# Performance work log

Measured on AMD Instinct MI355X. Metric: run time of the kernel, lower is better.

The kernel has to match this reference:

```python
import jax, jax.numpy as jnp
import numpy as np

B, L, D, H = 2, 2048, 2048, 16
C = D // H  # head dim = 128
EPS = 1e-5


def setup_inputs() -> dict:
    key = jax.random.key(0)
    k1, k2, k3, k4 = jax.random.split(key, 4)
    scale = 1.0 / np.sqrt(D)
    return {
        "x": jax.random.normal(k1, (B, L, D), dtype=jnp.float32),
        "theta": jax.random.uniform(k2, (B, L, D // 2), dtype=jnp.float32) * 6.2831853,
        "w_qkv": jax.random.normal(k3, (3 * D, D), dtype=jnp.float32) * scale,
        "w_y": jax.random.normal(k4, (D, D), dtype=jnp.float32) * scale,
        "b_y": jnp.zeros((D,), dtype=jnp.float32),
    }


def _rms_norm(t):
    # RMSNorm over last dim, eps=1e-5, no affine
    return t * jax.lax.rsqrt(jnp.mean(t * t, axis=-1, keepdims=True) + EPS)


def _apply_rope(q, k, theta):
    # q, k: (B, H, L, C); theta: (B, H, L, C//2)
    qr, qi = q[..., 0::2], q[..., 1::2]
    kr, ki = k[..., 0::2], k[..., 1::2]
    cos_t, sin_t = jnp.cos(theta), jnp.sin(theta)
    q_rot = jnp.stack((qr * cos_t - qi * sin_t, qr * sin_t + qi * cos_t), axis=-1).reshape(q.shape)
    k_rot = jnp.stack((kr * cos_t - ki * sin_t, kr * sin_t + ki * cos_t), axis=-1).reshape(k.shape)
    return q_rot, k_rot


def reference(x, theta, w_qkv, w_y, b_y):
    # QKV projection: (B, L, 3D)
    qkv = jnp.einsum("bld,ed->ble", x, w_qkv)
    # rearrange '... L (n H C) -> n ... H L C'
    qkv = qkv.reshape(B, L, 3, H, C).transpose(2, 0, 3, 1, 4)  # (3, B, H, L, C)
    q, k, v = qkv[0], qkv[1], qkv[2]
    q, k = _rms_norm(q), _rms_norm(k)
    # theta: (B, L, H*C/2) -> (B, H, L, C/2)
    th = theta.reshape(B, L, H, C // 2).transpose(0, 2, 1, 3)
    q, k = _apply_rope(q, k, th)
    # scaled dot-product attention
    scores = jnp.einsum("bhqc,bhkc->bhqk", q, k) / np.sqrt(C).astype(np.float32)
    attn = jax.nn.softmax(scores, axis=-1)
    y = jnp.einsum("bhqk,bhkc->bhqc", attn, v)
    # (B, H, L, C) -> (B, L, H*C)
    y = y.transpose(0, 2, 1, 3).reshape(B, L, D)
    return jnp.einsum("bld,ed->ble", y, w_y) + b_y
```

## Files before the change

kernel.cpp:

```cpp
#include <hip/hip_runtime.h>
#include <stdint.h>

typedef uint16_t u16;
typedef __attribute__((ext_vector_type(8))) short bf16x8;
typedef __attribute__((ext_vector_type(4))) float f32x4;


__device__ __forceinline__ u16 f2bf(float f) {
  uint32_t u = __builtin_bit_cast(uint32_t, f);
  u += 0x7fffu + ((u >> 16) & 1u);
  return (u16)(u >> 16);
}
__device__ __forceinline__ float bf2f(u16 h) {
  return __builtin_bit_cast(float, (uint32_t)h << 16);
}
__device__ __forceinline__ uint32_t pack2bf(float a, float b) {
  uint32_t ua = __builtin_bit_cast(uint32_t, a) + 0x7fffu;
  uint32_t ub = __builtin_bit_cast(uint32_t, b) + 0x7fffu;
  return (ua >> 16) | (ub & 0xffff0000u);
}
__device__ __forceinline__ void gl_lds16(const u16* g, u16* l) {
  __builtin_amdgcn_global_load_lds((const __attribute__((address_space(1))) uint32_t*)g,
                                   (__attribute__((address_space(3))) uint32_t*)l, 16, 0, 0);
}

__global__ __launch_bounds__(256) void cast3(const float* __restrict__ x,
                                             const float* __restrict__ wqkv,
                                             const float* __restrict__ wy,
                                             u16* __restrict__ xb, u16* __restrict__ wqb,
                                             u16* __restrict__ wyb) {
  const int N1 = 2097152, N2 = N1 + 3145728, N3 = N2 + 1048576;
  int stride = gridDim.x * 256;
  for (int i = blockIdx.x * 256 + threadIdx.x; i < N3; i += stride) {
    const float* src;
    u16* dst;
    int off;
    if (i < N1) {
      src = x; dst = xb; off = i;
    } else if (i < N2) {
      src = wqkv; dst = wqb; off = i - N1;
    } else {
      src = wy; dst = wyb; off = i - N2;
    }
    float4 v = *(const float4*)(src + (size_t)off * 4);
    uint32_t lo = (uint32_t)f2bf(v.x) | ((uint32_t)f2bf(v.y) << 16);
    uint32_t hi = (uint32_t)f2bf(v.z) | ((uint32_t)f2bf(v.w) << 16);
    *(uint2*)(dst + (size_t)off * 4) = make_uint2(lo, hi);
  }
}

__global__ __launch_bounds__(512, 1) void gemm8_qkv(
    const u16* __restrict__ A, const u16* __restrict__ Bw,
    u16* __restrict__ qb, u16* __restrict__ kb, u16* __restrict__ vt) {
  __shared__ u16 sm[57344];
  const int K = 2048;
  const int tid = threadIdx.x, lane = tid & 63;
  const int wid = tid >> 6, g = lane >> 4, lr = lane & 15;
  const int wm = wid >> 2, wn = wid & 3;
  const int m0 = blockIdx.y * 256, n0 = blockIdx.x * 192;
  const int srow = tid >> 3, sjs = (tid & 7) ^ (srow & 7);

  auto stA = [&](int buf, int kt, int R) {
    gl_lds16(A + (size_t)(m0 + R + srow) * K + kt * 64 + sjs * 8,
             &sm[buf * 28672 + R * 64 + tid * 8]);
  };
  auto stB = [&](int buf, int kt, int R) {
    gl_lds16(Bw + (size_t)(n0 + R + srow) * K + kt * 64 + sjs * 8,
             &sm[buf * 28672 + 16384 + R * 64 + tid * 8]);
  };
  auto rdA = [&](const u16* As, int mf, int ks) {
    int ra = wm * 128 + mf * 16 + lr;
    return *(const bf16x8*)&As[ra * 64 + (((ks * 4 + g) ^ (ra & 7)) * 8)];
  };
  auto rdB = [&](const u16* Bs, int nf, int ks) {
    int rb = wn * 48 + nf * 16 + lr;
    return *(const bf16x8*)&Bs[rb * 64 + (((ks * 4 + g) ^ (rb & 7)) * 8)];
  };

  f32x4 acc[8][3] = {};
  bf16x8 bc[3][2], fP0[4][2], fP1[4][2];

  stB(0, 0, 0); stB(0, 0, 64); stB(0, 0, 128);
  stA(0, 0, 0); stA(0, 0, 128);
  stA(0, 0, 64); stA(0, 0, 192);
  asm volatile("s_waitcnt vmcnt(2)" ::: "memory");
  __builtin_amdgcn_s_barrier();
  {
    const u16* As0 = &sm[0];
#pragma unroll
    for (int i = 0; i < 4; ++i)
#pragma unroll
      for (int ks = 0; ks < 2; ++ks) fP0[i][ks] = rdA(As0, i, ks);
  }

  for (int t = 0; t < 32; ++t) {
    const int cur = t & 1, nxt = cur ^ 1;
    const int kn = (t < 31) ? t + 1 : 31;
    const u16* Asc = &sm[cur * 28672];
    const u16* Bsc = &sm[cur * 28672 + 16384];
    const u16* Asn = &sm[nxt * 28672];

    stB(nxt, kn, 0); stB(nxt, kn, 64); stB(nxt, kn, 128);
    stA(nxt, kn, 0); stA(nxt, kn, 128);
    asm volatile("s_waitcnt vmcnt(5)" ::: "memory");
    __builtin_amdgcn_s_barrier();
#pragma unroll
    for (int nf = 0; nf < 3; ++nf)
#pragma unroll
      for (int ks = 0; ks < 2; ++ks) bc[nf][ks] = rdB(Bsc, nf, ks);
#pragma unroll
    for (int i = 0; i < 4; ++i)
#pragma unroll
      for (int ks = 0; ks < 2; ++ks) fP1[i][ks] = rdA(Asc, 4 + i, ks);
    __builtin_amdgcn_s_setprio(1);
#pragma unroll
    for (int i = 0; i < 4; ++i)
#pragma unroll
      for (int nf = 0; nf < 3; ++nf) {
        acc[i][nf] = __builtin_amdgcn_mfma_f32_16x16x32_bf16(
            fP0[i][0], bc[nf][0], acc[i][nf], 0, 0, 0);
        acc[i][nf] = __builtin_amdgcn_mfma_f32_16x16x32_bf16(
            fP0[i][1], bc[nf][1], acc[i][nf], 0, 0, 0);
      }
    __builtin_amdgcn_s_setprio(0);

    stA(nxt, kn, 64); stA(nxt, kn, 192);
    asm volatile("s_waitcnt vmcnt(2)" ::: "memory");
    __builtin_amdgcn_s_barrier();
#pragma unroll
    for (int i = 0; i < 4; ++i)
#pragma unroll
      for (int ks = 0; ks < 2; ++ks) fP0[i][ks] = rdA(Asn, i, ks);
    __builtin_amdgcn_s_setprio(1);
#pragma unroll
    for (int i = 0; i < 4; ++i)
#pragma unroll
      for (int nf = 0; nf < 3; ++nf) {
        acc[4 + i][nf] = __builtin_amdgcn_mfma_f32_16x16x32_bf16(
            fP1[i][0], bc[nf][0], acc[4 + i][nf], 0, 0, 0);
        acc[4 + i][nf] = __builtin_amdgcn_mfma_f32_16x16x32_bf16(
            fP1[i][1], bc[nf][1], acc[4 + i][nf], 0, 0, 0);
      }
    __builtin_amdgcn_s_setprio(0);
  }
  asm volatile("s_waitcnt vmcnt(0)" ::: "memory");

#pragma unroll
  for (int mf = 0; mf < 8; ++mf)
#pragma unroll
    for (int nf = 0; nf < 3; ++nf) {
      int n = n0 + wn * 48 + nf * 16 + lr;
      int s = n >> 11, h = (n >> 7) & 15, cb = n & 127;
#pragma unroll
      for (int r = 0; r < 4; ++r) {
        int m = m0 + wm * 128 + mf * 16 + g * 4 + r;
        int b = m >> 11, lp = m & 2047;
        u16 val = f2bf(acc[mf][nf][r]);
        if (s == 0)
          qb[(size_t)((b * 16 + h) * 2048 + lp) * 128 + cb] = val;
        else if (s == 1)
          kb[(size_t)((b * 16 + h) * 2048 + lp) * 128 + cb] = val;
        else
          vt[(size_t)((b * 16 + h) * 128 + cb) * 2048 + lp] = val;
      }
    }
}

__global__ __launch_bounds__(256, 2) void gemm_out(
    const u16* __restrict__ A, const u16* __restrict__ Bw,
    float* __restrict__ out, const float* __restrict__ bias) {
  __shared__ u16 sm[32768];
  const int K = 2048;
  const int tid = threadIdx.x, lane = tid & 63;
  const int wn = tid >> 6, g = lane >> 4, lr = lane & 15;
  const int m0 = blockIdx.y * 128, n0 = blockIdx.x * 128;
  const int srow = tid >> 3, sjs = (tid & 7) ^ (srow & 7);

  auto stA = [&](int buf, int kt, int R) {
    gl_lds16(A + (size_t)(m0 + R + srow) * K + kt * 64 + sjs * 8,
             &sm[buf * 16384 + R * 64 + tid * 8]);
  };
  auto stB = [&](int buf, int kt, int R) {
    gl_lds16(Bw + (size_t)(n0 + R + srow) * K + kt * 64 + sjs * 8,
             &sm[buf * 16384 + 8192 + R * 64 + tid * 8]);
  };
  auto rdA = [&](const u16* As, int mf, int ks) {
    int ra = mf * 16 + lr;
    return *(const bf16x8*)&As[ra * 64 + (((ks * 4 + g) ^ (ra & 7)) * 8)];
  };
  auto rdB = [&](const u16* Bs, int nf, int ks) {
    int rb = wn * 32 + nf * 16 + lr;
    return *(const bf16x8*)&Bs[rb * 64 + (((ks * 4 + g) ^ (rb & 7)) * 8)];
  };

  f32x4 acc[8][2] = {};
  bf16x8 bc[2][2], fP0[4][2], fP1[4][2];

  stB(0, 0, 0); stB(0, 0, 32); stB(0, 0, 64); stB(0, 0, 96);
  stA(0, 0, 0); stA(0, 0, 32);
  stA(0, 0, 64); stA(0, 0, 96);
  asm volatile("s_waitcnt vmcnt(2)" ::: "memory");
  __builtin_amdgcn_s_barrier();
  {
    const u16* As0 = &sm[0];
#pragma unroll
    for (int i = 0; i < 4; ++i)
#pragma unroll
      for (int ks = 0; ks < 2; ++ks) fP0[i][ks] = rdA(As0, i, ks);
  }

  for (int t = 0; t < 32; ++t) {
    const int cur = t & 1, nxt = cur ^ 1;
    const int kn = (t < 31) ? t + 1 : 31;
    const u16* Asc = &sm[cur * 16384];
    const u16* Bsc = &sm[cur * 16384 + 8192];
    const u16* Asn = &sm[nxt * 16384];

    stB(nxt, kn, 0); stB(nxt, kn, 32); stB(nxt, kn, 64); stB(nxt, kn, 96);
    stA(nxt, kn, 0); stA(nxt, kn, 32);
    asm volatile("s_waitcnt vmcnt(6)" ::: "memory");
    __builtin_amdgcn_s_barrier();
#pragma unroll
    for (int nf = 0; nf < 2; ++nf)
#pragma unroll
      for (int ks = 0; ks < 2; ++ks) bc[nf][ks] = rdB(Bsc, nf, ks);
#pragma unroll
    for (int i = 0; i < 4; ++i)
#pragma unroll
      for (int ks = 0; ks < 2; ++ks) fP1[i][ks] = rdA(Asc, 4 + i, ks);
    __builtin_amdgcn_s_setprio(1);
#pragma unroll
    for (int i = 0; i < 4; ++i)
#pragma unroll
      for (int nf = 0; nf < 2; ++nf) {
        acc[i][nf] = __builtin_amdgcn_mfma_f32_16x16x32_bf16(
            fP0[i][0], bc[nf][0], acc[i][nf], 0, 0, 0);
        acc[i][nf] = __builtin_amdgcn_mfma_f32_16x16x32_bf16(
            fP0[i][1], bc[nf][1], acc[i][nf], 0, 0, 0);
      }
    __builtin_amdgcn_s_setprio(0);

    stA(nxt, kn, 64); stA(nxt, kn, 96);
    asm volatile("s_waitcnt vmcnt(2)" ::: "memory");
    __builtin_amdgcn_s_barrier();
#pragma unroll
    for (int i = 0; i < 4; ++i)
#pragma unroll
      for (int ks = 0; ks < 2; ++ks) fP0[i][ks] = rdA(Asn, i, ks);
    __builtin_amdgcn_s_setprio(1);
#pragma unroll
    for (int i = 0; i < 4; ++i)
#pragma unroll
      for (int nf = 0; nf < 2; ++nf) {
        acc[4 + i][nf] = __builtin_amdgcn_mfma_f32_16x16x32_bf16(
            fP1[i][0], bc[nf][0], acc[4 + i][nf], 0, 0, 0);
        acc[4 + i][nf] = __builtin_amdgcn_mfma_f32_16x16x32_bf16(
            fP1[i][1], bc[nf][1], acc[4 + i][nf], 0, 0, 0);
      }
    __builtin_amdgcn_s_setprio(0);
  }
  asm volatile("s_waitcnt vmcnt(0)" ::: "memory");

#pragma unroll
  for (int mf = 0; mf < 8; ++mf)
#pragma unroll
    for (int nf = 0; nf < 2; ++nf) {
      int n = n0 + wn * 32 + nf * 16 + lr;
      float bv = bias[n];
#pragma unroll
      for (int r = 0; r < 4; ++r) {
        int m = m0 + mf * 16 + g * 4 + r;
        out[(size_t)m * 2048 + n] = acc[mf][nf][r] + bv;
      }
    }
}

__global__ __launch_bounds__(256) void k_fix(u16* __restrict__ kb,
                                             const float* __restrict__ theta) {
  const int row = blockIdx.x * 4 + (threadIdx.x >> 6);
  const int lane = threadIdx.x & 63;
  const int bh = row >> 11, l = row & 2047;
  const int b = bh >> 4, h = bh & 15;
  float th = theta[(size_t)(b * 2048 + l) * 1024 + h * 64 + lane];
  float sn, cs;
  __sincosf(th, &sn, &cs);
  uint32_t* p = (uint32_t*)(kb + (size_t)row * 128) + lane;
  uint32_t v = *p;
  float x0 = bf2f((u16)(v & 0xffff)), x1 = bf2f((u16)(v >> 16));
  float ss = x0 * x0 + x1 * x1;
#pragma unroll
  for (int m = 1; m <= 32; m <<= 1) ss += __shfl_xor(ss, m);
  float rn = rsqrtf(ss * (1.0f / 128.0f) + 1e-5f);
  x0 *= rn;
  x1 *= rn;
  float y0 = x0 * cs - x1 * sn;
  float y1 = x0 * sn + x1 * cs;
  *p = (uint32_t)f2bf(y0) | ((uint32_t)f2bf(y1) << 16);
}

__global__ __launch_bounds__(512, 1) void attn_k(const u16* __restrict__ qb,
                                                 const u16* __restrict__ kb,
                                                 const u16* __restrict__ vt,
                                                 const float* __restrict__ theta,
                                                 u16* __restrict__ yb) {
  __shared__ u16 sm[49152];
  const int gid = blockIdx.x;
  const int bh = (gid & 7) * 4 + ((gid >> 3) & 3);
  const int qtile = gid >> 5;
  const int b = bh >> 4, h = bh & 15;
  const int tid = threadIdx.x, lane = tid & 63, wid = tid >> 6;
  const int g = lane >> 4, lr = lane & 15;
  const int q0 = qtile * 256 + wid * 32;

  bf16x8 qf[2][4];
#pragma unroll
  for (int qs = 0; qs < 2; ++qs) {
    const int l = q0 + qs * 16 + lr;
    const u16* qrow = qb + (size_t)(bh * 2048 + l) * 128;
    float ss = 0.f;
#pragma unroll
    for (int ks = 0; ks < 4; ++ks) {
      bf16x8 raw = *(const bf16x8*)&qrow[ks * 32 + g * 8];
#pragma unroll
      for (int e = 0; e < 8; ++e) {
        float xv = bf2f((u16)raw[e]);
        ss += xv * xv;
      }
    }
    ss += __shfl_xor(ss, 16);
    ss += __shfl_xor(ss, 32);
    float rn = rsqrtf(ss * (1.0f / 128.0f) + 1e-5f) * 0.12751743f;
    const float* thp = theta + (size_t)(b * 2048 + l) * 1024 + h * 64;
#pragma unroll
    for (int ks = 0; ks < 4; ++ks) {
      bf16x8 raw = *(const bf16x8*)&qrow[ks * 32 + g * 8];
      float4 th4 = *(const float4*)&thp[ks * 16 + g * 4];
      union {
        uint32_t u[4];
        bf16x8 v;
      } outv;
#pragma unroll
      for (int j = 0; j < 4; ++j) {
        float th = (&th4.x)[j];
        float sn, cs;
        __sincosf(th, &sn, &cs);
        float x0 = bf2f((u16)raw[2 * j]) * rn;
        float x1 = bf2f((u16)raw[2 * j + 1]) * rn;
        outv.u[j] = pack2bf(x0 * cs - x1 * sn, x0 * sn + x1 * cs);
      }
      qf[qs][ks] = outv.v;
    }
  }

  auto stage = [&](int buf, int kv) {
#pragma unroll
    for (int i = 0; i < 2; ++i) {
      int ci = i * 512 + tid;
      int row = ci >> 4, j = ci & 15;
      gl_lds16(kb + (size_t)(bh * 2048 + kv + row) * 128 + (j ^ (row & 7)) * 8,
               &sm[buf * 8192 + ci * 8]);
    }
#pragma unroll
    for (int i = 0; i < 2; ++i) {
      int ci = i * 512 + tid;
      int row = ci >> 3, j = ci & 7;
      gl_lds16(vt + (size_t)(bh * 128 + row) * 2048 + kv + (j ^ (row & 7)) * 8,
               &sm[24576 + buf * 8192 + ci * 8]);
    }
  };

  f32x4 acc[2][8] = {};
  float mrun[2] = {-1e30f, -1e30f}, lrun[2] = {0.f, 0.f};
  const int sA = (2 * (g & 1)) * 16 + lr, sB = sA + 16;
  const bool hi2 = (g >> 1) != 0;

  stage(0, 0);
  stage(1, 64);
  asm volatile("s_waitcnt vmcnt(4)" ::: "memory");
  __builtin_amdgcn_s_barrier();

  int cur = 0;
  for (int t = 0; t < 32; ++t) {
    if (t < 31) {
      int nb = (cur == 0) ? 2 : cur - 1;
      int kvn = ((t < 30) ? t + 2 : 31) * 64;
      stage(nb, kvn);
    }
    const u16* Ks = &sm[cur * 8192];
    const u16* Vs = &sm[24576 + cur * 8192];

    f32x4 st[2][4] = {};
#pragma unroll
    for (int ks = 0; ks < 4; ++ks) {
      bf16x8 kf[4];
#pragma unroll
      for (int kt = 0; kt < 4; ++kt) {
        int row = kt * 16 + lr;
        kf[kt] = *(const bf16x8*)&Ks[row * 128 + (((ks * 4 + g) ^ (row & 7)) * 8)];
      }
#pragma unroll
      for (int kt = 0; kt < 4; ++kt)
#pragma unroll
        for (int qs = 0; qs < 2; ++qs)
          st[qs][kt] =
              __builtin_amdgcn_mfma_f32_16x16x32_bf16(kf[kt], qf[qs][ks], st[qs][kt], 0, 0, 0);
    }

    float pmax[2];
#pragma unroll
    for (int qs = 0; qs < 2; ++qs) {
      float m01 = fmaxf(fmaxf(st[qs][0][0], st[qs][0][1]), fmaxf(st[qs][0][2], st[qs][0][3]));
      float m23 = fmaxf(fmaxf(st[qs][1][0], st[qs][1][1]), fmaxf(st[qs][1][2], st[qs][1][3]));
      float m45 = fmaxf(fmaxf(st[qs][2][0], st[qs][2][1]), fmaxf(st[qs][2][2], st[qs][2][3]));
      float m67 = fmaxf(fmaxf(st[qs][3][0], st[qs][3][1]), fmaxf(st[qs][3][2], st[qs][3][3]));
      float mx = fmaxf(fmaxf(m01, m23), fmaxf(m45, m67));
      mx = fmaxf(mx, __shfl_xor(mx, 16));
      mx = fmaxf(mx, __shfl_xor(mx, 32));
      pmax[qs] = mx;
    }
    float need = fmaxf(pmax[0] - mrun[0], pmax[1] - mrun[1]);
    if (!__all(need <= 8.0f)) {
#pragma unroll
      for (int qs = 0; qs < 2; ++qs) {
        float mnew = fmaxf(mrun[qs], pmax[qs]);
        float corr = __builtin_amdgcn_exp2f(mrun[qs] - mnew);
        lrun[qs] *= corr;
        mrun[qs] = mnew;
#pragma unroll
        for (int ct = 0; ct < 8; ++ct) {
          acc[qs][ct][0] *= corr;
          acc[qs][ct][1] *= corr;
          acc[qs][ct][2] *= corr;
          acc[qs][ct][3] *= corr;
        }
      }
    }
    uint32_t pw[2][4][2];
#pragma unroll
    for (int qs = 0; qs < 2; ++qs) {
      float rsum = 0.f;
#pragma unroll
      for (int kt = 0; kt < 4; ++kt)
#pragma unroll
        for (int hf = 0; hf < 2; ++hf) {
          float e0 = __builtin_amdgcn_exp2f(st[qs][kt][2 * hf] - mrun[qs]);
          float e1 = __builtin_amdgcn_exp2f(st[qs][kt][2 * hf + 1] - mrun[qs]);
          rsum += e0 + e1;
          pw[qs][kt][hf] = pack2bf(e0, e1);
        }
      rsum += __shfl_xor(rsum, 16);
      rsum += __shfl_xor(rsum, 32);
      lrun[qs] += rsum;
    }

#pragma unroll
    for (int ks2 = 0; ks2 < 2; ++ks2) {
      bf16x8 pf[2];
#pragma unroll
      for (int qs = 0; qs < 2; ++qs) {
        uint32_t a0 = __shfl(pw[qs][ks2 * 2][0], sA);
        uint32_t a1 = __shfl(pw[qs][ks2 * 2][1], sA);
        uint32_t a2 = __shfl(pw[qs][ks2 * 2][0], sB);
        uint32_t a3 = __shfl(pw[qs][ks2 * 2][1], sB);
        uint32_t b0 = __shfl(pw[qs][ks2 * 2 + 1][0], sA);
        uint32_t b1 = __shfl(pw[qs][ks2 * 2 + 1][1], sA);
        uint32_t b2 = __shfl(pw[qs][ks2 * 2 + 1][0], sB);
        uint32_t b3 = __shfl(pw[qs][ks2 * 2 + 1][1], sB);
        union {
          uint32_t u[4];
          bf16x8 v;
        } tt;
        tt.u[0] = hi2 ? b0 : a0;
        tt.u[1] = hi2 ? b1 : a1;
        tt.u[2] = hi2 ? b2 : a2;
        tt.u[3] = hi2 ? b3 : a3;
        pf[qs] = tt.v;
      }
#pragma unroll
      for (int ct = 0; ct < 8; ++ct) {
        int row = ct * 16 + lr;
        bf16x8 vf = *(const bf16x8*)&Vs[row * 64 + (((ks2 * 4 + g) ^ (row & 7)) * 8)];
#pragma unroll
        for (int qs = 0; qs < 2; ++qs)
          acc[qs][ct] = __builtin_amdgcn_mfma_f32_16x16x32_bf16(vf, pf[qs], acc[qs][ct], 0, 0, 0);
      }
    }
    if (t < 31) {
      asm volatile("s_waitcnt vmcnt(4)" ::: "memory");
      __builtin_amdgcn_s_barrier();
    }
    cur = (cur == 2) ? 0 : cur + 1;
  }
  asm volatile("s_waitcnt vmcnt(0)" ::: "memory");

#pragma unroll
  for (int qs = 0; qs < 2; ++qs) {
    float inv = 1.f / lrun[qs];
    const size_t orow = (size_t)(b * 2048 + q0 + qs * 16 + lr) * 2048 + h * 128;
#pragma unroll
    for (int ct = 0; ct < 8; ++ct) {
      uint32_t lo = pack2bf(acc[qs][ct][0] * inv, acc[qs][ct][1] * inv);
      uint32_t hi = pack2bf(acc[qs][ct][2] * inv, acc[qs][ct][3] * inv);
      *(uint2*)&yb[orow + ct * 16 + g * 4] = make_uint2(lo, hi);
    }
  }
}

extern "C" void kernel_launch(void* const* d_in, const int* in_sizes, int n_in,
                              void* d_out, int out_size, void* d_ws, size_t ws_size,
                              hipStream_t stream) {
  const float* x = (const float*)d_in[0];
  const float* theta = (const float*)d_in[1];
  const float* wqkv = (const float*)d_in[2];
  const float* wy = (const float*)d_in[3];
  const float* by = (const float*)d_in[4];
  float* out = (float*)d_out;
  char* ws = (char*)d_ws;
  u16* xb  = (u16*)(ws + 0);
  u16* wqb = (u16*)(ws + 16777216);
  u16* wyb = (u16*)(ws + 41943040);
  u16* qb  = (u16*)(ws + 50331648);
  u16* kb  = (u16*)(ws + 67108864);
  u16* vt  = (u16*)(ws + 83886080);
  u16* yb  = (u16*)(ws + 100663296);

  cast3<<<2048, 256, 0, stream>>>(x, wqkv, wy, xb, wqb, wyb);
  gemm8_qkv<<<dim3(32, 16), 512, 0, stream>>>(xb, wqb, qb, kb, vt);
  k_fix<<<16384, 256, 0, stream>>>(kb, theta);
  attn_k<<<256, 512, 0, stream>>>(qb, kb, vt, theta, yb);
  gemm_out<<<dim3(16, 32), 256, 0, stream>>>(yb, wyb, out, by);
}
```

Before: 280.5 us.

## Halve attention query tile per block to double grid and occupancy

Each wave in the attention kernel now handles 16 query rows instead of 32, so a block covers 128 queries and the grid grows from 256 to 512 blocks. Launch bounds now allow two blocks per CU, and per-wave accumulator and score registers are halved. This is meant to fill all CUs and hide latency, but each K/V tile staged into LDS now feeds half as many MFMAs, which doubles K/V global and LDS traffic per unit of compute. Shared memory of 96KB per block may also limit whether two blocks actually fit on one CU.

New measurement: 301.1 us. +7.3%, slower.

```diff
diff --git a/kernel.cpp b/kernel.cpp
--- a/kernel.cpp
+++ b/kernel.cpp
@@ -298,7 +298,7 @@
   *p = (uint32_t)f2bf(y0) | ((uint32_t)f2bf(y1) << 16);
 }
 
-__global__ __launch_bounds__(512, 1) void attn_k(const u16* __restrict__ qb,
+__global__ __launch_bounds__(512, 2) void attn_k(const u16* __restrict__ qb,
                                                  const u16* __restrict__ kb,
                                                  const u16* __restrict__ vt,
                                                  const float* __restrict__ theta,
@@ -310,12 +310,11 @@
   const int b = bh >> 4, h = bh & 15;
   const int tid = threadIdx.x, lane = tid & 63, wid = tid >> 6;
   const int g = lane >> 4, lr = lane & 15;
-  const int q0 = qtile * 256 + wid * 32;
-
-  bf16x8 qf[2][4];
-#pragma unroll
-  for (int qs = 0; qs < 2; ++qs) {
-    const int l = q0 + qs * 16 + lr;
+  const int q0 = qtile * 128 + wid * 16;
+
+  bf16x8 qf[4];
+  {
+    const int l = q0 + lr;
     const u16* qrow = qb + (size_t)(bh * 2048 + l) * 128;
     float ss = 0.f;
 #pragma unroll
@@ -348,7 +347,7 @@
         float x1 = bf2f((u16)raw[2 * j + 1]) * rn;
         outv.u[j] = pack2bf(x0 * cs - x1 * sn, x0 * sn + x1 * cs);
       }
-      qf[qs][ks] = outv.v;
+      qf[ks] = outv.v;
     }
   }
 
@@ -369,8 +368,8 @@
     }
   };
 
-  f32x4 acc[2][8] = {};
-  float mrun[2] = {-1e30f, -1e30f}, lrun[2] = {0.f, 0.f};
+  f32x4 acc[8] = {};
+  float mrun = -1e30f, lrun = 0.f;
   const int sA = (2 * (g & 1)) * 16 + lr, sB = sA + 16;
   const bool hi2 = (g >> 1) != 0;
 
@@ -389,7 +388,7 @@
     const u16* Ks = &sm[cur * 8192];
     const u16* Vs = &sm[24576 + cur * 8192];
 
-    f32x4 st[2][4] = {};
+    f32x4 st[4] = {};
 #pragma unroll
     for (int ks = 0; ks < 4; ++ks) {
       bf16x8 kf[4];
@@ -400,89 +399,67 @@
       }
 #pragma unroll
       for (int kt = 0; kt < 4; ++kt)
-#pragma unroll
-        for (int qs = 0; qs < 2; ++qs)
-          st[qs][kt] =
-              __builtin_amdgcn_mfma_f32_16x16x32_bf16(kf[kt], qf[qs][ks], st[qs][kt], 0, 0, 0);
-    }
-
-    float pmax[2];
-#pragma unroll
-    for (int qs = 0; qs < 2; ++qs) {
-      float m01 = fmaxf(fmaxf(st[qs][0][0], st[qs][0][1]), fmaxf(st[qs][0][2], st[qs][0][3]));
-      float m23 = fmaxf(fmaxf(st[qs][1][0], st[qs][1][1]), fmaxf(st[qs][1][2], st[qs][1][3]));
-      float m45 = fmaxf(fmaxf(st[qs][2][0], st[qs][2][1]), fmaxf(st[qs][2][2], st[qs][2][3]));
-      float m67 = fmaxf(fmaxf(st[qs][3][0], st[qs][3][1]), fmaxf(st[qs][3][2], st[qs][3][3]));
-      float mx = fmaxf(fmaxf(m01, m23), fmaxf(m45, m67));
-      mx = fmaxf(mx, __shfl_xor(mx, 16));
-      mx = fmaxf(mx, __shfl_xor(mx, 32));
-      pmax[qs] = mx;
-    }
-    float need = fmaxf(pmax[0] - mrun[0], pmax[1] - mrun[1]);
-    if (!__all(need <= 8.0f)) {
-#pragma unroll
-      for (int qs = 0; qs < 2; ++qs) {
-        float mnew = fmaxf(mrun[qs], pmax[qs]);
-        float corr = __builtin_amdgcn_exp2f(mrun[qs] - mnew);
-        lrun[qs] *= corr;
-        mrun[qs] = mnew;
-#pragma unroll
-        for (int ct = 0; ct < 8; ++ct) {
-          acc[qs][ct][0] *= corr;
-          acc[qs][ct][1] *= corr;
-          acc[qs][ct][2] *= corr;
-          acc[qs][ct][3] *= corr;
-        }
-      }
-    }
-    uint32_t pw[2][4][2];
-#pragma unroll
-    for (int qs = 0; qs < 2; ++qs) {
-      float rsum = 0.f;
-#pragma unroll
-      for (int kt = 0; kt < 4; ++kt)
-#pragma unroll
-        for (int hf = 0; hf < 2; ++hf) {
-          float e0 = __builtin_amdgcn_exp2f(st[qs][kt][2 * hf] - mrun[qs]);
-          float e1 = __builtin_amdgcn_exp2f(st[qs][kt][2 * hf + 1] - mrun[qs]);
-          rsum += e0 + e1;
-          pw[qs][kt][hf] = pack2bf(e0, e1);
-        }
-      rsum += __shfl_xor(rsum, 16);
-      rsum += __shfl_xor(rsum, 32);
-      lrun[qs] += rsum;
-    }
+        st[kt] = __builtin_amdgcn_mfma_f32_16x16x32_bf16(kf[kt], qf[ks], st[kt], 0, 0, 0);
+    }
+
+    float m01 = fmaxf(fmaxf(st[0][0], st[0][1]), fmaxf(st[0][2], st[0][3]));
+    float m23 = fmaxf(fmaxf(st[1][0], st[1][1]), fmaxf(st[1][2], st[1][3]));
+    float m45 = fmaxf(fmaxf(st[2][0], st[2][1]), fmaxf(st[2][2], st[2][3]));
+    float m67 = fmaxf(fmaxf(st[3][0], st[3][1]), fmaxf(st[3][2], st[3][3]));
+    float pmax = fmaxf(fmaxf(m01, m23), fmaxf(m45, m67));
+    pmax = fmaxf(pmax, __shfl_xor(pmax, 16));
+    pmax = fmaxf(pmax, __shfl_xor(pmax, 32));
+    if (!__all(pmax - mrun <= 8.0f)) {
+      float mnew = fmaxf(mrun, pmax);
+      float corr = __builtin_amdgcn_exp2f(mrun - mnew);
+      lrun *= corr;
+      mrun = mnew;
+#pragma unroll
+      for (int ct = 0; ct < 8; ++ct) {
+        acc[ct][0] *= corr;
+        acc[ct][1] *= corr;
+        acc[ct][2] *= corr;
+        acc[ct][3] *= corr;
+      }
+    }
+    uint32_t pw[4][2];
+    float rsum = 0.f;
+#pragma unroll
+    for (int kt = 0; kt < 4; ++kt)
+#pragma unroll
+      for (int hf = 0; hf < 2; ++hf) {
+        float e0 = __builtin_amdgcn_exp2f(st[kt][2 * hf] - mrun);
+        float e1 = __builtin_amdgcn_exp2f(st[kt][2 * hf + 1] - mrun);
+        rsum += e0 + e1;
+        pw[kt][hf] = pack2bf(e0, e1);
+      }
+    rsum += __shfl_xor(rsum, 16);
+    rsum += __shfl_xor(rsum, 32);
+    lrun += rsum;
 
 #pragma unroll
     for (int ks2 = 0; ks2 < 2; ++ks2) {
-      bf16x8 pf[2];
-#pragma unroll
-      for (int qs = 0; qs < 2; ++qs) {
-        uint32_t a0 = __shfl(pw[qs][ks2 * 2][0], sA);
-        uint32_t a1 = __shfl(pw[qs][ks2 * 2][1], sA);
-        uint32_t a2 = __shfl(pw[qs][ks2 * 2][0], sB);
-        uint32_t a3 = __shfl(pw[qs][ks2 * 2][1], sB);
-        uint32_t b0 = __shfl(pw[qs][ks2 * 2 + 1][0], sA);
-        uint32_t b1 = __shfl(pw[qs][ks2 * 2 + 1][1], sA);
-        uint32_t b2 = __shfl(pw[qs][ks2 * 2 + 1][0], sB);
-        uint32_t b3 = __shfl(pw[qs][ks2 * 2 + 1][1], sB);
-        union {
-          uint32_t u[4];
-          bf16x8 v;
-        } tt;
-        tt.u[0] = hi2 ? b0 : a0;
-        tt.u[1] = hi2 ? b1 : a1;
-        tt.u[2] = hi2 ? b2 : a2;
-        tt.u[3] = hi2 ? b3 : a3;
-        pf[qs] = tt.v;
-      }
+      uint32_t a0 = __shfl(pw[ks2 * 2][0], sA);
+      uint32_t a1 = __shfl(pw[ks2 * 2][1], sA);
+      uint32_t a2 = __shfl(pw[ks2 * 2][0], sB);
+      uint32_t a3 = __shfl(pw[ks2 * 2][1], sB);
+      uint32_t b0 = __shfl(pw[ks2 * 2 + 1][0], sA);
+      uint32_t b1 = __shfl(pw[ks2 * 2 + 1][1], sA);
+      uint32_t b2 = __shfl(pw[ks2 * 2 + 1][0], sB);
+      uint32_t b3 = __shfl(pw[ks2 * 2 + 1][1], sB);
+      union {
+        uint32_t u[4];
+        bf16x8 v;
+      } tt;
+      tt.u[0] = hi2 ? b0 : a0;
+      tt.u[1] = hi2 ? b1 : a1;
+      tt.u[2] = hi2 ? b2 : a2;
+      tt.u[3] = hi2 ? b3 : a3;
 #pragma unroll
       for (int ct = 0; ct < 8; ++ct) {
         int row = ct * 16 + lr;
         bf16x8 vf = *(const bf16x8*)&Vs[row * 64 + (((ks2 * 4 + g) ^ (row & 7)) * 8)];
-#pragma unroll
-        for (int qs = 0; qs < 2; ++qs)
-          acc[qs][ct] = __builtin_amdgcn_mfma_f32_16x16x32_bf16(vf, pf[qs], acc[qs][ct], 0, 0, 0);
+        acc[ct] = __builtin_amdgcn_mfma_f32_16x16x32_bf16(vf, tt.v, acc[ct], 0, 0, 0);
       }
     }
     if (t < 31) {
@@ -493,14 +470,13 @@
   }
   asm volatile("s_waitcnt vmcnt(0)" ::: "memory");
 
-#pragma unroll
-  for (int qs = 0; qs < 2; ++qs) {
-    float inv = 1.f / lrun[qs];
-    const size_t orow = (size_t)(b * 2048 + q0 + qs * 16 + lr) * 2048 + h * 128;
+  {
+    float inv = 1.f / lrun;
+    const size_t orow = (size_t)(b * 2048 + q0 + lr) * 2048 + h * 128;
 #pragma unroll
     for (int ct = 0; ct < 8; ++ct) {
-      uint32_t lo = pack2bf(acc[qs][ct][0] * inv, acc[qs][ct][1] * inv);
-      uint32_t hi = pack2bf(acc[qs][ct][2] * inv, acc[qs][ct][3] * inv);
+      uint32_t lo = pack2bf(acc[ct][0] * inv, acc[ct][1] * inv);
+      uint32_t hi = pack2bf(acc[ct][2] * inv, acc[ct][3] * inv);
       *(uint2*)&yb[orow + ct * 16 + g * 4] = make_uint2(lo, hi);
     }
   }
@@ -527,6 +503,6 @@
   cast3<<<2048, 256, 0, stream>>>(x, wqkv, wy, xb, wqb, wyb);
   gemm8_qkv<<<dim3(32, 16), 512, 0, stream>>>(xb, wqb, qb, kb, vt);
   k_fix<<<16384, 256, 0, stream>>>(kb, theta);
-  attn_k<<<256, 512, 0, stream>>>(qb, kb, vt, theta, yb);
+  attn_k<<<512, 512, 0, stream>>>(qb, kb, vt, theta, yb);
   gemm_out<<<dim3(16, 32), 256, 0, stream>>>(yb, wyb, out, by);
 }
```
